# Kernel optimization log

Measured on AMD Instinct MI355X. Metric: run time of the kernel, lower is better.

Reference implementation:

```python
import jax, jax.numpy as jnp
import numpy as np

G, T, D_IN, D_OUT = 8, 4096, 1024, 4096


def setup_inputs() -> dict:
    key = jax.random.key(0)
    k1, k2, k3 = jax.random.split(key, 3)
    x = jax.random.normal(k1, (T, D_IN), dtype=jnp.float32)
    # cumulative end offsets per group: sorted, last == T (grouped_mm convention)
    cuts = jnp.sort(jax.random.randint(k2, (G - 1,), 0, T, dtype=jnp.int32))
    offs = jnp.concatenate([cuts, jnp.array([T], dtype=jnp.int32)])
    weight = jax.random.normal(k3, (G, D_OUT, D_IN), dtype=jnp.float32) * (D_IN ** -0.5)
    return {"input": x, "grouped_mm_offs": offs, "weight": weight}


def reference(input, grouped_mm_offs, weight):
    # Grouped GEMM: row t (with offs[g-1] <= t < offs[g]) -> input[t] @ weight[g].T
    n_tok = input.shape[0]
    tok = jnp.arange(n_tok)
    gid = jnp.searchsorted(grouped_mm_offs, tok, side="right")  # [T] group id per row
    # Dense all-expert projection [G, T, D_OUT], then select the routed expert per row.
    proj = jnp.einsum("ti,goi->gto", input, weight)
    return proj[gid, tok]  # [T, D_OUT]
```

## Files before the change

### kernel.cpp

```cpp
#include <hip/hip_runtime.h>
#include <hip/hip_bf16.h>

#define NG 8
#define NT 4096
#define DIN 1024
#define DOUT 4096
#define BM 128
#define BN 128
#define BK 64
#define KTILES (DIN / BK)
#define NTILES (DOUT / BN)
#define RTILES (NT / BM + NG)
#define ATILESZ (BM * BK * 2)
#define BTILESZ (BN * BK * 2)

typedef __attribute__((ext_vector_type(4))) float f32x4;
typedef __attribute__((ext_vector_type(8))) short bf16x8;

__device__ __forceinline__ void gld16(const void* g, void* l) {
    __builtin_amdgcn_global_load_lds(
        (const __attribute__((address_space(1))) void*)(g),
        (__attribute__((address_space(3))) void*)(l), 16, 0, 0);
}

__device__ __forceinline__ unsigned long long pack4bf(f32x4 v) {
    union { __hip_bfloat16 h; unsigned short u; } c0, c1, c2, c3;
    c0.h = __float2bfloat16(v[0]);
    c1.h = __float2bfloat16(v[1]);
    c2.h = __float2bfloat16(v[2]);
    c3.h = __float2bfloat16(v[3]);
    return (unsigned long long)c0.u | ((unsigned long long)c1.u << 16) |
           ((unsigned long long)c2.u << 32) | ((unsigned long long)c3.u << 48);
}

__device__ __forceinline__ int swz(int row, int colb) {
    return row * 128 + (colb ^ ((row & 7) << 4));
}

__global__ __launch_bounds__(256)
void cvt_x_kernel(const float* __restrict__ x, short* __restrict__ xb) {
    const int n4 = NT * DIN / 4;
    for (int i = blockIdx.x * blockDim.x + threadIdx.x; i < n4;
         i += gridDim.x * blockDim.x) {
        f32x4 v = ((const f32x4*)x)[i];
        ((unsigned long long*)xb)[i] = pack4bf(v);
    }
}

__global__ __launch_bounds__(256, 2)
void grouped_gemm_bf16(const short* __restrict__ xb,
                       const int* __restrict__ offs,
                       const float* __restrict__ w,
                       float* __restrict__ out) {
    __shared__ char lds[2 * ATILESZ + BTILESZ];
    char* ldsA = lds;
    char* ldsB = lds + 2 * ATILESZ;

    const int rt = blockIdx.y;
    const int n0 = blockIdx.x * BN;
    int row0 = 0, endg = 0, gsel = -1;
    {
        int acc0 = 0, prev = 0;
        for (int g = 0; g < NG; ++g) {
            int e = offs[g];
            int cnt = (e - prev + BM - 1) / BM;
            if (rt < acc0 + cnt) { gsel = g; row0 = prev + (rt - acc0) * BM; endg = e; break; }
            acc0 += cnt; prev = e;
        }
    }
    if (gsel < 0) return;
    const float* wg = w + (size_t)gsel * DOUT * DIN;

    const int tid  = threadIdx.x;
    const int lane = tid & 63;
    const int wid  = tid >> 6;
    const int wr   = wid >> 1, wc = wid & 1;
    const int lrow = lane & 15, kgrp = lane >> 4;

    int axoff[4], sbaseA[4];
    #pragma unroll
    for (int i = 0; i < 4; ++i) {
        int stripe = i * 4 + wid;
        int r = stripe * 8 + (lane >> 3);
        int cs = (lane & 7) ^ (r & 7);
        int ar = row0 + r; if (ar >= endg) ar = endg - 1;
        axoff[i]  = ar * DIN + cs * 8;
        sbaseA[i] = stripe * 1024;
    }
    const int sr = tid >> 4, sc4 = tid & 15;
    int boff[8];
    #pragma unroll
    for (int i = 0; i < 8; ++i) boff[i] = (n0 + sr + i * 16) * DIN + sc4 * 4;

    f32x4 acc[4][4];
    #pragma unroll
    for (int m = 0; m < 4; ++m)
        #pragma unroll
        for (int n = 0; n < 4; ++n)
            acc[m][n] = (f32x4){0.f, 0.f, 0.f, 0.f};

    f32x4 pB[8];

    #pragma unroll
    for (int i = 0; i < 8; ++i) pB[i] = *(const f32x4*)(wg + boff[i]);
    #pragma unroll
    for (int i = 0; i < 4; ++i) gld16(xb + axoff[i], ldsA + sbaseA[i]);
    #pragma unroll
    for (int i = 0; i < 8; ++i)
        *(unsigned long long*)(ldsB + swz(sr + i * 16, sc4 * 8)) = pack4bf(pB[i]);

    for (int kt = 0; kt < KTILES; ++kt) {
        const int cur = kt & 1;
        const char* lA = ldsA + cur * ATILESZ;

        if (kt + 1 < KTILES) {
            const int k0 = (kt + 1) * BK;
            #pragma unroll
            for (int i = 0; i < 8; ++i) pB[i] = *(const f32x4*)(wg + boff[i] + k0);
            #pragma unroll
            for (int i = 0; i < 4; ++i)
                gld16(xb + axoff[i] + k0, ldsA + (cur ^ 1) * ATILESZ + sbaseA[i]);
            __builtin_amdgcn_sched_barrier(0);
            asm volatile("s_waitcnt vmcnt(12) lgkmcnt(0)" ::: "memory");
        } else {
            __builtin_amdgcn_sched_barrier(0);
            asm volatile("s_waitcnt vmcnt(0) lgkmcnt(0)" ::: "memory");
        }
        __builtin_amdgcn_sched_barrier(0);
        __builtin_amdgcn_s_barrier();
        __builtin_amdgcn_sched_barrier(0);

        __builtin_amdgcn_s_setprio(1);
        #pragma unroll
        for (int kk = 0; kk < 2; ++kk) {
            const int kb = kk * 64 + kgrp * 16;
            bf16x8 af[4], bb[4];
            #pragma unroll
            for (int m = 0; m < 4; ++m) {
                int r = wr * 64 + m * 16 + lrow;
                af[m] = *(const bf16x8*)(lA + r * 128 + (((kb >> 4) ^ (r & 7)) << 4));
            }
            #pragma unroll
            for (int n = 0; n < 4; ++n)
                bb[n] = *(const bf16x8*)(ldsB + swz(wc * 64 + n * 16 + lrow, kb));
            #pragma unroll
            for (int m = 0; m < 4; ++m)
                #pragma unroll
                for (int n = 0; n < 4; ++n)
                    acc[m][n] = __builtin_amdgcn_mfma_f32_16x16x32_bf16(
                        af[m], bb[n], acc[m][n], 0, 0, 0);
        }
        __builtin_amdgcn_s_setprio(0);

        if (kt + 1 < KTILES) {
            __builtin_amdgcn_sched_barrier(0);
            __builtin_amdgcn_s_barrier();
            __builtin_amdgcn_sched_barrier(0);
            #pragma unroll
            for (int i = 0; i < 8; ++i)
                *(unsigned long long*)(ldsB + swz(sr + i * 16, sc4 * 8)) = pack4bf(pB[i]);
        }
    }

    #pragma unroll
    for (int m = 0; m < 4; ++m) {
        #pragma unroll
        for (int j = 0; j < 4; ++j) {
            int row = row0 + wr * 64 + m * 16 + kgrp * 4 + j;
            if (row < endg) {
                #pragma unroll
                for (int n = 0; n < 4; ++n) {
                    int col = n0 + wc * 64 + n * 16 + lrow;
                    out[(size_t)row * DOUT + col] = acc[m][n][j];
                }
            }
        }
    }
}

extern "C" void kernel_launch(void* const* d_in, const int* in_sizes, int n_in,
                              void* d_out, int out_size, void* d_ws, size_t ws_size,
                              hipStream_t stream) {
    const float* x    = (const float*)d_in[0];
    const int*   offs = (const int*)d_in[1];
    const float* w    = (const float*)d_in[2];
    float* out = (float*)d_out;
    short* xb  = (short*)d_ws;

    cvt_x_kernel<<<1024, 256, 0, stream>>>(x, xb);
    dim3 grid(NTILES, RTILES, 1);
    grouped_gemm_bf16<<<grid, 256, 0, stream>>>(xb, offs, w, out);
}
```

Before: 71.25 us.

## Deepen weight prefetch to two k-tiles with double-buffered LDS B tile

Fp32 weight tiles are now prefetched two k-steps ahead, using two register buffers that alternate. The LDS B tile is also double-buffered, and the k loop is unrolled by two through a macro so that buffer indices are compile-time constants. The wait counts are adjusted so each step waits only for the A tile it needs while the weight loads stay in flight. This aims to hide global-memory latency on the weight stream better, at the cost of about 32 extra VGPRs and twice the LDS for B. That could hurt occupancy at two blocks per CU.

```diff
diff --git a/kernel.cpp b/kernel.cpp
--- a/kernel.cpp
+++ b/kernel.cpp
@@ -47,12 +47,70 @@
     }
 }
 
+#define KSTEP(KT, AR, AW, BR, BW, PBI, PBC)                                      \
+  {                                                                              \
+    if ((KT) + 1 < KTILES) {                                                     \
+      const int k0a = ((KT) + 1) * BK;                                           \
+      _Pragma("unroll")                                                          \
+      for (int i = 0; i < 4; ++i)                                                \
+        gld16(xb + axoff[i] + k0a, ldsA + (AW) * ATILESZ + sbaseA[i]);           \
+      __builtin_amdgcn_sched_barrier(0);                                         \
+    }                                                                            \
+    if ((KT) + 2 < KTILES) {                                                     \
+      const int k0b = ((KT) + 2) * BK;                                           \
+      _Pragma("unroll")                                                          \
+      for (int i = 0; i < 8; ++i) PBI[i] = *(const f32x4*)(wg + boff[i] + k0b);  \
+      __builtin_amdgcn_sched_barrier(0);                                         \
+    }                                                                            \
+    if ((KT) + 2 < KTILES)                                                       \
+      asm volatile("s_waitcnt vmcnt(20) lgkmcnt(0)" ::: "memory");               \
+    else if ((KT) + 1 < KTILES)                                                  \
+      asm volatile("s_waitcnt vmcnt(12) lgkmcnt(0)" ::: "memory");               \
+    else                                                                         \
+      asm volatile("s_waitcnt vmcnt(0) lgkmcnt(0)" ::: "memory");                \
+    __builtin_amdgcn_sched_barrier(0);                                           \
+    __builtin_amdgcn_s_barrier();      \
+    __builtin_amdgcn_sched_barrier(0);                                           \
+    __builtin_amdgcn_s_setprio(1);                                               \
+    _Pragma("unroll")                                                            \
+    for (int kk = 0; kk < 2; ++kk) {                                             \
+      const int kb = kk * 64 + kgrp * 16;                                        \
+      bf16x8 af[4], bb[4];                                                       \
+      _Pragma("unroll")                                                          \
+      for (int m = 0; m < 4; ++m) {                                              \
+        int r = wr * 64 + m * 16 + lrow;                                         \
+        af[m] = *(const bf16x8*)(ldsA + (AR) * ATILESZ + r * 128 +               \
+                                 (((kb >> 4) ^ (r & 7)) << 4));                  \
+      }                                                                          \
+      _Pragma("unroll")                                                          \
+      for (int n = 0; n < 4; ++n)                                                \
+        bb[n] = *(const bf16x8*)(ldsB + (BR) * BTILESZ +                         \
+                                 swz(wc * 64 + n * 16 + lrow, kb));              \
+      _Pragma("unroll")                                                          \
+      for (int m = 0; m < 4; ++m)                                                \
+        _Pragma("unroll")                                                        \
+        for (int n = 0; n < 4; ++n)                                              \
+          acc[m][n] = __builtin_amdgcn_mfma_f32_16x16x32_bf16(                   \
+              af[m], bb[n], acc[m][n], 0, 0, 0);                                 \
+    }                                                                            \
+    __builtin_amdgcn_s_setprio(0);                                               \
+    if ((KT) + 1 < KTILES) {                                                     \
+      __builtin_amdgcn_sched_barrier(0);                                         \
+      __builtin_amdgcn_s_barrier();     \
+      __builtin_amdgcn_sched_barrier(0);                                         \
+      _Pragma("unroll")                                                          \
+      for (int i = 0; i < 8; ++i)      \
+        *(unsigned long long*)(ldsB + (BW) * BTILESZ +                           \
+                               swz(sr + i * 16, sc4 * 8)) = pack4bf(PBC[i]);     \
+    }                                                                            \
+  }
+
 __global__ __launch_bounds__(256, 2)
 void grouped_gemm_bf16(const short* __restrict__ xb,
                        const int* __restrict__ offs,
                        const float* __restrict__ w,
                        float* __restrict__ out) {
-    __shared__ char lds[2 * ATILESZ + BTILESZ];
+    __shared__ char lds[2 * ATILESZ + 2 * BTILESZ];
     char* ldsA = lds;
     char* ldsB = lds + 2 * ATILESZ;
 
@@ -99,67 +157,25 @@
         for (int n = 0; n < 4; ++n)
             acc[m][n] = (f32x4){0.f, 0.f, 0.f, 0.f};
 
-    f32x4 pB[8];
-
-    #pragma unroll
-    for (int i = 0; i < 8; ++i) pB[i] = *(const f32x4*)(wg + boff[i]);
+    f32x4 pBa[8], pBb[8];
+
+    #pragma unroll
+    for (int i = 0; i < 8; ++i) pBa[i] = *(const f32x4*)(wg + boff[i]);
+    __builtin_amdgcn_sched_barrier(0);
     #pragma unroll
     for (int i = 0; i < 4; ++i) gld16(xb + axoff[i], ldsA + sbaseA[i]);
+    __builtin_amdgcn_sched_barrier(0);
+    #pragma unroll
+    for (int i = 0; i < 8; ++i) pBb[i] = *(const f32x4*)(wg + boff[i] + BK);
+    __builtin_amdgcn_sched_barrier(0);
     #pragma unroll
     for (int i = 0; i < 8; ++i)
-        *(unsigned long long*)(ldsB + swz(sr + i * 16, sc4 * 8)) = pack4bf(pB[i]);
-
-    for (int kt = 0; kt < KTILES; ++kt) {
-        const int cur = kt & 1;
-        const char* lA = ldsA + cur * ATILESZ;
-
-        if (kt + 1 < KTILES) {
-            const int k0 = (kt + 1) * BK;
-            #pragma unroll
-            for (int i = 0; i < 8; ++i) pB[i] = *(const f32x4*)(wg + boff[i] + k0);
-            #pragma unroll
-            for (int i = 0; i < 4; ++i)
-                gld16(xb + axoff[i] + k0, ldsA + (cur ^ 1) * ATILESZ + sbaseA[i]);
-            __builtin_amdgcn_sched_barrier(0);
-            asm volatile("s_waitcnt vmcnt(12) lgkmcnt(0)" ::: "memory");
-        } else {
-            __builtin_amdgcn_sched_barrier(0);
-            asm volatile("s_waitcnt vmcnt(0) lgkmcnt(0)" ::: "memory");
-        }
-        __builtin_amdgcn_sched_barrier(0);
-        __builtin_amdgcn_s_barrier();
-        __builtin_amdgcn_sched_barrier(0);
-
-        __builtin_amdgcn_s_setprio(1);
-        #pragma unroll
-        for (int kk = 0; kk < 2; ++kk) {
-            const int kb = kk * 64 + kgrp * 16;
-            bf16x8 af[4], bb[4];
-            #pragma unroll
-            for (int m = 0; m < 4; ++m) {
-                int r = wr * 64 + m * 16 + lrow;
-                af[m] = *(const bf16x8*)(lA + r * 128 + (((kb >> 4) ^ (r & 7)) << 4));
-            }
-            #pragma unroll
-            for (int n = 0; n < 4; ++n)
-                bb[n] = *(const bf16x8*)(ldsB + swz(wc * 64 + n * 16 + lrow, kb));
-            #pragma unroll
-            for (int m = 0; m < 4; ++m)
-                #pragma unroll
-                for (int n = 0; n < 4; ++n)
-                    acc[m][n] = __builtin_amdgcn_mfma_f32_16x16x32_bf16(
-                        af[m], bb[n], acc[m][n], 0, 0, 0);
-        }
-        __builtin_amdgcn_s_setprio(0);
-
-        if (kt + 1 < KTILES) {
-            __builtin_amdgcn_sched_barrier(0);
-            __builtin_amdgcn_s_barrier();
-            __builtin_amdgcn_sched_barrier(0);
-            #pragma unroll
-            for (int i = 0; i < 8; ++i)
-                *(unsigned long long*)(ldsB + swz(sr + i * 16, sc4 * 8)) = pack4bf(pB[i]);
-        }
+        *(unsigned long long*)(ldsB + swz(sr + i * 16, sc4 * 8)) = pack4bf(pBa[i]);
+
+    for (int k2 = 0; k2 < 8; ++k2) {
+        const int kte = 2 * k2;
+        KSTEP(kte,     0, 1, 0, 1, pBa, pBb);
+        KSTEP(kte + 1, 1, 0, 1, 0, pBb, pBa);
     }
 
     #pragma unroll
```

Result: slower. 79.21 us (+11.2%).

## Process two 128-row A halves per block to reuse each converted B tile

Applied to the files above, without the earlier changes.

Each block now covers 256 rows instead of 128, computing two 128x128 output tiles that share one bf16-converted weight tile in LDS. A three-slot rotating A buffer interleaves the loads of the two row halves with their MFMA phases, with added barriers between the phases. This halves the redundant fp32 weight loads and their bf16 conversions per output. In exchange it doubles the accumulator registers (which may cut occupancy below two blocks per CU), wastes more work on padded tiles for small groups, and launches fewer blocks.

```diff
diff --git a/kernel.cpp b/kernel.cpp
--- a/kernel.cpp
+++ b/kernel.cpp
@@ -5,13 +5,13 @@
 #define NT 4096
 #define DIN 1024
 #define DOUT 4096
-#define BM 128
+#define BMP 256
 #define BN 128
 #define BK 64
 #define KTILES (DIN / BK)
 #define NTILES (DOUT / BN)
-#define RTILES (NT / BM + NG)
-#define ATILESZ (BM * BK * 2)
+#define RTILES (NT / BMP + NG)
+#define ATILESZ (128 * BK * 2)
 #define BTILESZ (BN * BK * 2)
 
 typedef __attribute__((ext_vector_type(4))) float f32x4;
@@ -52,9 +52,9 @@
                        const int* __restrict__ offs,
                        const float* __restrict__ w,
                        float* __restrict__ out) {
-    __shared__ char lds[2 * ATILESZ + BTILESZ];
+    __shared__ char lds[3 * ATILESZ + BTILESZ];
     char* ldsA = lds;
-    char* ldsB = lds + 2 * ATILESZ;
+    char* ldsB = lds + 3 * ATILESZ;
 
     const int rt = blockIdx.y;
     const int n0 = blockIdx.x * BN;
@@ -63,8 +63,8 @@
         int acc0 = 0, prev = 0;
         for (int g = 0; g < NG; ++g) {
             int e = offs[g];
-            int cnt = (e - prev + BM - 1) / BM;
-            if (rt < acc0 + cnt) { gsel = g; row0 = prev + (rt - acc0) * BM; endg = e; break; }
+            int cnt = (e - prev + BMP - 1) / BMP;
+            if (rt < acc0 + cnt) { gsel = g; row0 = prev + (rt - acc0) * BMP; endg = e; break; }
             acc0 += cnt; prev = e;
         }
     }
@@ -77,14 +77,16 @@
     const int wr   = wid >> 1, wc = wid & 1;
     const int lrow = lane & 15, kgrp = lane >> 4;
 
-    int axoff[4], sbaseA[4];
+    int axoff0[4], axoff1[4], sbaseA[4];
     #pragma unroll
     for (int i = 0; i < 4; ++i) {
         int stripe = i * 4 + wid;
         int r = stripe * 8 + (lane >> 3);
         int cs = (lane & 7) ^ (r & 7);
-        int ar = row0 + r; if (ar >= endg) ar = endg - 1;
-        axoff[i]  = ar * DIN + cs * 8;
+        int a0 = row0 + r;        if (a0 >= endg) a0 = endg - 1;
+        int a1 = row0 + 128 + r;  if (a1 >= endg) a1 = endg - 1;
+        axoff0[i] = a0 * DIN + cs * 8;
+        axoff1[i] = a1 * DIN + cs * 8;
         sbaseA[i] = stripe * 1024;
     }
     const int sr = tid >> 4, sc4 = tid & 15;
@@ -92,65 +94,111 @@
     #pragma unroll
     for (int i = 0; i < 8; ++i) boff[i] = (n0 + sr + i * 16) * DIN + sc4 * 4;
 
-    f32x4 acc[4][4];
+    f32x4 acc0[4][4], acc1[4][4];
     #pragma unroll
     for (int m = 0; m < 4; ++m)
         #pragma unroll
-        for (int n = 0; n < 4; ++n)
-            acc[m][n] = (f32x4){0.f, 0.f, 0.f, 0.f};
+        for (int n = 0; n < 4; ++n) {
+            acc0[m][n] = (f32x4){0.f, 0.f, 0.f, 0.f};
+            acc1[m][n] = (f32x4){0.f, 0.f, 0.f, 0.f};
+        }
 
     f32x4 pB[8];
 
     #pragma unroll
     for (int i = 0; i < 8; ++i) pB[i] = *(const f32x4*)(wg + boff[i]);
     #pragma unroll
-    for (int i = 0; i < 4; ++i) gld16(xb + axoff[i], ldsA + sbaseA[i]);
+    for (int i = 0; i < 4; ++i) gld16(xb + axoff0[i], ldsA + sbaseA[i]);
+    #pragma unroll
+    for (int i = 0; i < 4; ++i) gld16(xb + axoff1[i], ldsA + ATILESZ + sbaseA[i]);
     #pragma unroll
     for (int i = 0; i < 8; ++i)
         *(unsigned long long*)(ldsB + swz(sr + i * 16, sc4 * 8)) = pack4bf(pB[i]);
 
+    int bufc = 0;
+
     for (int kt = 0; kt < KTILES; ++kt) {
-        const int cur = kt & 1;
-        const char* lA = ldsA + cur * ATILESZ;
-
+        const int b0 = bufc;
+        const int b1 = (bufc + 1 == 3) ? 0 : bufc + 1;
+        const int b2 = (b1 + 1 == 3) ? 0 : b1 + 1;
+
+        asm volatile("s_waitcnt vmcnt(4) lgkmcnt(0)" ::: "memory");
+        __builtin_amdgcn_sched_barrier(0);
+        __builtin_amdgcn_s_barrier();
+        __builtin_amdgcn_sched_barrier(0);
         if (kt + 1 < KTILES) {
             const int k0 = (kt + 1) * BK;
             #pragma unroll
             for (int i = 0; i < 8; ++i) pB[i] = *(const f32x4*)(wg + boff[i] + k0);
+            __builtin_amdgcn_sched_barrier(0);
             #pragma unroll
             for (int i = 0; i < 4; ++i)
-                gld16(xb + axoff[i] + k0, ldsA + (cur ^ 1) * ATILESZ + sbaseA[i]);
-            __builtin_amdgcn_sched_barrier(0);
-            asm volatile("s_waitcnt vmcnt(12) lgkmcnt(0)" ::: "memory");
-        } else {
-            __builtin_amdgcn_sched_barrier(0);
-            asm volatile("s_waitcnt vmcnt(0) lgkmcnt(0)" ::: "memory");
-        }
+                gld16(xb + axoff0[i] + k0, ldsA + b2 * ATILESZ + sbaseA[i]);
+            __builtin_amdgcn_sched_barrier(0);
+        }
+        {
+            const char* lA = ldsA + b0 * ATILESZ;
+            __builtin_amdgcn_s_setprio(1);
+            #pragma unroll
+            for (int kk = 0; kk < 2; ++kk) {
+                const int kb = kk * 64 + kgrp * 16;
+                bf16x8 af[4], bb[4];
+                #pragma unroll
+                for (int m = 0; m < 4; ++m) {
+                    int r = wr * 64 + m * 16 + lrow;
+                    af[m] = *(const bf16x8*)(lA + r * 128 + (((kb >> 4) ^ (r & 7)) << 4));
+                }
+                #pragma unroll
+                for (int n = 0; n < 4; ++n)
+                    bb[n] = *(const bf16x8*)(ldsB + swz(wc * 64 + n * 16 + lrow, kb));
+                #pragma unroll
+                for (int m = 0; m < 4; ++m)
+                    #pragma unroll
+                    for (int n = 0; n < 4; ++n)
+                        acc0[m][n] = __builtin_amdgcn_mfma_f32_16x16x32_bf16(
+                            af[m], bb[n], acc0[m][n], 0, 0, 0);
+            }
+            __builtin_amdgcn_s_setprio(0);
+        }
+
+        if (kt + 1 < KTILES)
+            asm volatile("s_waitcnt vmcnt(12)" ::: "memory");
+        else
+            asm volatile("s_waitcnt vmcnt(0)" ::: "memory");
         __builtin_amdgcn_sched_barrier(0);
         __builtin_amdgcn_s_barrier();
         __builtin_amdgcn_sched_barrier(0);
-
-        __builtin_amdgcn_s_setprio(1);
-        #pragma unroll
-        for (int kk = 0; kk < 2; ++kk) {
-            const int kb = kk * 64 + kgrp * 16;
-            bf16x8 af[4], bb[4];
-            #pragma unroll
-            for (int m = 0; m < 4; ++m) {
-                int r = wr * 64 + m * 16 + lrow;
-                af[m] = *(const bf16x8*)(lA + r * 128 + (((kb >> 4) ^ (r & 7)) << 4));
-            }
-            #pragma unroll
-            for (int n = 0; n < 4; ++n)
-                bb[n] = *(const bf16x8*)(ldsB + swz(wc * 64 + n * 16 + lrow, kb));
-            #pragma unroll
-            for (int m = 0; m < 4; ++m)
+        if (kt + 1 < KTILES) {
+            const int k0 = (kt + 1) * BK;
+            #pragma unroll
+            for (int i = 0; i < 4; ++i)
+                gld16(xb + axoff1[i] + k0, ldsA + b0 * ATILESZ + sbaseA[i]);
+            __builtin_amdgcn_sched_barrier(0);
+        }
+        {
+            const char* lA = ldsA + b1 * ATILESZ;
+            __builtin_amdgcn_s_setprio(1);
+            #pragma unroll
+            for (int kk = 0; kk < 2; ++kk) {
+                const int kb = kk * 64 + kgrp * 16;
+                bf16x8 af[4], bb[4];
+                #pragma unroll
+                for (int m = 0; m < 4; ++m) {
+                    int r = wr * 64 + m * 16 + lrow;
+                    af[m] = *(const bf16x8*)(lA + r * 128 + (((kb >> 4) ^ (r & 7)) << 4));
+                }
                 #pragma unroll
                 for (int n = 0; n < 4; ++n)
-                    acc[m][n] = __builtin_amdgcn_mfma_f32_16x16x32_bf16(
-                        af[m], bb[n], acc[m][n], 0, 0, 0);
-        }
-        __builtin_amdgcn_s_setprio(0);
+                    bb[n] = *(const bf16x8*)(ldsB + swz(wc * 64 + n * 16 + lrow, kb));
+                #pragma unroll
+                for (int m = 0; m < 4; ++m)
+                    #pragma unroll
+                    for (int n = 0; n < 4; ++n)
+                        acc1[m][n] = __builtin_amdgcn_mfma_f32_16x16x32_bf16(
+                            af[m], bb[n], acc1[m][n], 0, 0, 0);
+            }
+            __builtin_amdgcn_s_setprio(0);
+        }
 
         if (kt + 1 < KTILES) {
             __builtin_amdgcn_sched_barrier(0);
@@ -160,18 +208,27 @@
             for (int i = 0; i < 8; ++i)
                 *(unsigned long long*)(ldsB + swz(sr + i * 16, sc4 * 8)) = pack4bf(pB[i]);
         }
+        bufc = b2;
     }
 
     #pragma unroll
     for (int m = 0; m < 4; ++m) {
         #pragma unroll
         for (int j = 0; j < 4; ++j) {
-            int row = row0 + wr * 64 + m * 16 + kgrp * 4 + j;
-            if (row < endg) {
+            int r0 = row0 + wr * 64 + m * 16 + kgrp * 4 + j;
+            if (r0 < endg) {
                 #pragma unroll
                 for (int n = 0; n < 4; ++n) {
                     int col = n0 + wc * 64 + n * 16 + lrow;
-                    out[(size_t)row * DOUT + col] = acc[m][n][j];
+                    out[(size_t)r0 * DOUT + col] = acc0[m][n][j];
+                }
+            }
+            int r1 = r0 + 128;
+            if (r1 < endg) {
+                #pragma unroll
+                for (int n = 0; n < 4; ++n) {
+                    int col = n0 + wc * 64 + n * 16 + lrow;
+                    out[(size_t)r1 * DOUT + col] = acc1[m][n][j];
                 }
             }
         }
```

Measured after the change: 76.86 us. +7.9%, slower.
